# Kernel optimization log

Measured on AMD Instinct MI355X. Metric: run time of the kernel, lower is better.

The kernel has to match this reference:

```python
import jax, jax.numpy as jnp
import numpy as np


def _ln(x, g, b, eps=1e-5):
    m = x.mean(-1, keepdims=True)
    v = x.var(-1, keepdims=True)
    return (x - m) / jnp.sqrt(v + eps) * g + b


def setup_inputs() -> dict:
    key = jax.random.key(0)
    ks = iter(jax.random.split(key, 48))
    B, N, H, Ld, L, FF = 2048, 10, 256, 8, 4, 1024
    def w(shape, s=0.02):
        return jax.random.normal(next(ks), shape, jnp.float32) * s
    return dict(
        latent_code=jax.random.normal(next(ks), (B, Ld), jnp.float32),
        target_node_types=jax.random.randint(next(ks), (B, N), 0, 5),
        ce_w1=w((Ld, H)), ce_b1=jnp.zeros(H), ce_g1=jnp.ones(H), ce_be1=jnp.zeros(H),
        ce_w2=w((H, H)), ce_b2=jnp.zeros(H), ce_g2=jnp.ones(H), ce_be2=jnp.zeros(H),
        nc_w1=w((2, H // 4)), nc_b1=jnp.zeros(H // 4), nc_w2=w((H // 4, 3)), nc_b2=jnp.zeros(3),
        type_emb=w((5, H), 1.0), pos_emb=w((N, H), 0.02),
        qkvo_w=w((L, 4, H, H)), qkvo_b=jnp.zeros((L, 4, H)),
        ln_g=jnp.ones((L, 2, H)), ln_b=jnp.zeros((L, 2, H)),
        ffn_w1=w((L, H, FF)), ffn_b1=jnp.zeros((L, FF)),
        ffn_w2=w((L, FF, H)), ffn_b2=jnp.zeros((L, H)),
        out_w=w((H, 5)), out_b=jnp.zeros(5),
        edge_w1=w((2 * H + Ld, H)), edge_b1=jnp.zeros(H),
        edge_w2=w((H, 8)), edge_b2=jnp.zeros(8),
    )


def reference(latent_code, target_node_types,
              ce_w1, ce_b1, ce_g1, ce_be1, ce_w2, ce_b2, ce_g2, ce_be2,
              nc_w1, nc_b1, nc_w2, nc_b2,
              type_emb, pos_emb, qkvo_w, qkvo_b, ln_g, ln_b,
              ffn_w1, ffn_b1, ffn_w2, ffn_b2, out_w, out_b,
              edge_w1, edge_b1, edge_w2, edge_b2):
    B, Ld = latent_code.shape
    N = target_node_types.shape[1]
    H = ce_w1.shape[1]
    L = qkvo_w.shape[0]
    nh = 8
    hd = H // nh

    # context encoder: Linear -> LN -> ReLU -> Linear -> LN
    h0 = jax.nn.relu(_ln(latent_code @ ce_w1 + ce_b1, ce_g1, ce_be1))
    context = _ln(h0 @ ce_w2 + ce_b2, ce_g2, ce_be2)  # [B,H]

    # node count head on latent_code[:, :2]
    node_count_logits = jax.nn.relu(latent_code[:, :2] @ nc_w1 + nc_b1) @ nc_w2 + nc_b2  # [B,3]

    # teacher-forced node embeddings (independent of predictions -> vectorizable)
    ne = type_emb[target_node_types] + pos_emb[:N]          # [B,N,H]
    h = context[:, None, :] + pos_emb[:N]                   # queries [B,N,H]
    mem = jnp.concatenate([context[:, None, :], ne], axis=1)  # keys [B,N+1,H]
    # position i attends to context (k=0) and nodes j<i (k=j+1), i.e. k <= i
    kmask = (jnp.arange(N + 1)[None, :] <= jnp.arange(N)[:, None])  # [N,N+1]
    scale = 1.0 / np.sqrt(hd).astype(np.float32)

    for l in range(L):
        Q = (h @ qkvo_w[l, 0] + qkvo_b[l, 0]).reshape(B, N, nh, hd)
        K = (mem @ qkvo_w[l, 1] + qkvo_b[l, 1]).reshape(B, N + 1, nh, hd)
        V = (mem @ qkvo_w[l, 2] + qkvo_b[l, 2]).reshape(B, N + 1, nh, hd)
        s = jnp.einsum('bnhd,bmhd->bhnm', Q, K) * scale
        s = jnp.where(kmask[None, None], s, jnp.float32(-1e9))
        a = jax.nn.softmax(s, axis=-1)
        o = jnp.einsum('bhnm,bmhd->bnhd', a, V).reshape(B, N, H)
        h = _ln(h + o @ qkvo_w[l, 3] + qkvo_b[l, 3], ln_g[l, 0], ln_b[l, 0])
        f = jax.nn.relu(h @ ffn_w1[l] + ffn_b1[l]) @ ffn_w2[l] + ffn_b2[l]
        h = _ln(h + f, ln_g[l, 1], ln_b[l, 1])

    node_logits = h @ out_w + out_b  # [B,N,5]

    # pairwise edge decoder on (emb_i, emb_j, latent) for i>j, symmetrized
    ei = jnp.broadcast_to(ne[:, :, None, :], (B, N, N, H))
    ej = jnp.broadcast_to(ne[:, None, :, :], (B, N, N, H))
    lat = jnp.broadcast_to(latent_code[:, None, None, :], (B, N, N, Ld))
    feat = jnp.concatenate([ei, ej, lat], axis=-1)  # [B,N,N,2H+Ld]
    elog = jax.nn.relu(feat @ edge_w1 + edge_b1) @ edge_w2 + edge_b2  # [B,N,N,8]
    tril = (jnp.arange(N)[:, None] > jnp.arange(N)[None, :])[None, :, :, None]
    lower = jnp.where(tril, elog, jnp.float32(0.0))
    edge_component_logits = lower + jnp.swapaxes(lower, 1, 2)  # diag stays zero

    return node_logits, node_count_logits, edge_component_logits
```

## Files before the change

### kernel.cpp

```cpp
#include <hip/hip_runtime.h>
#include <hip/hip_bf16.h>

#define BATCH 2048
#define NNODE 10
#define NLAYER 4
#define ROWS_H (BATCH*NNODE)
#define ROWS_M (BATCH*(NNODE+1))
#define KVSTR 2048

typedef __hip_bfloat16 bf16;
typedef unsigned short u16;
typedef unsigned int u32;
typedef __attribute__((ext_vector_type(8))) short bf16x8;
typedef __attribute__((ext_vector_type(4))) float f32x4;

__device__ __forceinline__ float bfb(u16 u) {
    union { u32 i; float f; } c; c.i = (u32)u << 16; return c.f;
}
__device__ __forceinline__ float bf2f(bf16 x) { return __bfloat162float(x); }
__device__ __forceinline__ bf16 f2bf(float x) { return __float2bfloat16(x); }
__device__ __forceinline__ u16 f2u(float v) {
    bf16 t = f2bf(v); u16 u; __builtin_memcpy(&u, &t, 2); return u;
}
__device__ __forceinline__ void store_out(void* out, int f32o, size_t idx, float v) {
    if (f32o) ((float*)out)[idx] = v; else ((bf16*)out)[idx] = f2bf(v);
}
__device__ __forceinline__ int dflag(const u32* g) { return g[0] == 0x3F800000u; }

#define GLL(src, dst) __builtin_amdgcn_global_load_lds( \
    (const __attribute__((address_space(1))) void*)(src), \
    (__attribute__((address_space(3))) void*)(dst), 16, 0, 0)

#define NT 26
struct CvtArgs { const void* src[NT]; int n[NT]; int off[NT]; };

__global__ __launch_bounds__(256) void cvt_kernel(CvtArgs a, bf16* __restrict__ dst,
                                                  const u32* __restrict__ gptr) {
    int f = dflag(gptr);
    int gid = blockIdx.x * 256 + threadIdx.x;
    int stride = gridDim.x * 256;
    for (int tn = 0; tn < NT; tn++) {
        const void* s = a.src[tn];
        bf16* d = dst + a.off[tn];
        int n = a.n[tn];
        if (f) {
            const float* sf = (const float*)s;
            for (int i = gid; i < n; i += stride) d[i] = f2bf(sf[i]);
        } else {
            const bf16* sb = (const bf16*)s;
            for (int i = gid; i < n; i += stride) d[i] = sb[i];
        }
    }
}

#define NTT 26
struct TTArgs {
    const void* src[NTT];
    int soff[NTT]; int doff[NTT]; int R[NTT]; int C[NTT];
    int tileStart[NTT];
    int nTiles;
};

__global__ __launch_bounds__(256) void tt_kernel(TTArgs a, u16* __restrict__ dst,
                                                 const u32* __restrict__ gptr) {
    int f = dflag(gptr);
    int bid = blockIdx.x;
    if (bid >= a.nTiles) return;
    int tn = 0;
    while (tn + 1 < NTT && a.tileStart[tn + 1] <= bid) tn++;
    int lt = bid - a.tileStart[tn];
    int R = a.R[tn], C = a.C[tn];
    int tilesC = C >> 6;
    int tr = lt / tilesC, tc = lt - tr * tilesC;

    __shared__ u16 Ts[64 * 66];
    int t = threadIdx.x;

    if (f) {
        const float* s = (const float*)a.src[tn] + a.soff[tn];
        #pragma unroll
        for (int it = 0; it < 16; it++) {
            int flat = it * 256 + t;
            int lr = flat >> 6, lc = flat & 63;
            Ts[lr * 66 + lc] = f2u(s[(size_t)(tr * 64 + lr) * C + tc * 64 + lc]);
        }
    } else {
        const u16* s = (const u16*)a.src[tn] + a.soff[tn];
        #pragma unroll
        for (int it = 0; it < 16; it++) {
            int flat = it * 256 + t;
            int lr = flat >> 6, lc = flat & 63;
            Ts[lr * 66 + lc] = s[(size_t)(tr * 64 + lr) * C + tc * 64 + lc];
        }
    }
    __syncthreads();

    u16* d = dst + a.doff[tn];
    #pragma unroll
    for (int it = 0; it < 16; it++) {
        int flat = it * 256 + t;
        int orow = flat >> 6, ocol = flat & 63;
        d[(size_t)(tc * 64 + orow) * R + tr * 64 + ocol] = Ts[ocol * 66 + orow];
    }
}

__global__ __launch_bounds__(256) void kvbias_kernel(const bf16* __restrict__ qb,
                                                     bf16* __restrict__ dst) {
    int t = blockIdx.x * 256 + threadIdx.x;
    if (t < 2048) {
        int l = t >> 9, c = t & 511;
        dst[t] = qb[(l * 4 + 1) * 256 + c];
    }
}

__device__ __forceinline__ void ln_stats256(float x, float* s_red, float& m, float& var) {
    float v1 = x, v2 = x * x;
    #pragma unroll
    for (int off = 32; off; off >>= 1) {
        v1 += __shfl_down(v1, off, 64);
        v2 += __shfl_down(v2, off, 64);
    }
    int wave = threadIdx.x >> 6, lane = threadIdx.x & 63;
    if (!lane) { s_red[wave] = v1; s_red[4 + wave] = v2; }
    __syncthreads();
    m   = (s_red[0] + s_red[1] + s_red[2] + s_red[3]) * (1.f / 256.f);
    var = (s_red[4] + s_red[5] + s_red[6] + s_red[7]) * (1.f / 256.f) - m * m;
    __syncthreads();
}

__global__ __launch_bounds__(256) void ctx_kernel(
    const bf16* __restrict__ lat_bf, const int* __restrict__ types,
    const bf16* __restrict__ ce_w1, const bf16* __restrict__ ce_b1,
    const bf16* __restrict__ ce_g1, const bf16* __restrict__ ce_be1,
    const bf16* __restrict__ ce_w2, const bf16* __restrict__ ce_b2,
    const bf16* __restrict__ ce_g2, const bf16* __restrict__ ce_be2,
    const bf16* __restrict__ nc_w1, const bf16* __restrict__ nc_b1,
    const bf16* __restrict__ nc_w2, const bf16* __restrict__ nc_b2,
    const bf16* __restrict__ type_emb, const bf16* __restrict__ pos_emb,
    const bf16* __restrict__ edge_w1, const bf16* __restrict__ edge_b1,
    bf16* __restrict__ h, bf16* __restrict__ mem, bf16* __restrict__ ne,
    bf16* __restrict__ rvec, void* __restrict__ out, const u32* __restrict__ gptr)
{
    int b = blockIdx.x;
    int t = threadIdx.x;
    int f32o = dflag(gptr);
    __shared__ float lat[8];
    __shared__ float s_h0[256];
    __shared__ float s_red[8];
    __shared__ float s_nc[64];

    if (t < 8) lat[t] = bf2f(lat_bf[b * 8 + t]);
    __syncthreads();

    float x = bf2f(ce_b1[t]);
    #pragma unroll
    for (int k = 0; k < 8; k++) x += lat[k] * bf2f(ce_w1[k * 256 + t]);
    float m, var;
    ln_stats256(x, s_red, m, var);
    float r = rsqrtf(var + 1e-5f);
    float h0 = fmaxf((x - m) * r * bf2f(ce_g1[t]) + bf2f(ce_be1[t]), 0.f);
    s_h0[t] = h0;
    __syncthreads();

    float x2 = bf2f(ce_b2[t]);
    for (int k = 0; k < 256; k++) x2 += s_h0[k] * bf2f(ce_w2[k * 256 + t]);
    ln_stats256(x2, s_red, m, var);
    r = rsqrtf(var + 1e-5f);
    float ctx = (x2 - m) * r * bf2f(ce_g2[t]) + bf2f(ce_be2[t]);

    mem[(size_t)(b * 11) * 256 + t] = f2bf(ctx);
    for (int n = 0; n < NNODE; n++) {
        float pe = bf2f(pos_emb[n * 256 + t]);
        h[(size_t)(b * NNODE + n) * 256 + t] = f2bf(ctx + pe);
        int ty = types[b * NNODE + n];
        float nv = bf2f(type_emb[ty * 256 + t]) + pe;
        ne[(size_t)(b * NNODE + n) * 256 + t] = f2bf(nv);
        mem[(size_t)(b * 11 + 1 + n) * 256 + t] = f2bf(nv);
    }

    float rv = bf2f(edge_b1[t]);
    #pragma unroll
    for (int k = 0; k < 8; k++) rv += lat[k] * bf2f(edge_w1[(512 + k) * 256 + t]);
    rvec[(size_t)b * 256 + t] = f2bf(rv);

    if (t < 64) {
        float hn = lat[0] * bf2f(nc_w1[t]) + lat[1] * bf2f(nc_w1[64 + t]) + bf2f(nc_b1[t]);
        s_nc[t] = fmaxf(hn, 0.f);
    }
    __syncthreads();
    if (t < 3) {
        float o = bf2f(nc_b2[t]);
        for (int k = 0; k < 64; k++) o += s_nc[k] * bf2f(nc_w2[k * 3 + t]);
        store_out(out, f32o, (size_t)102400 + b * 3 + t, o);
    }
}

__global__ __launch_bounds__(256) void gemm_mfma(
    const u16* __restrict__ A, const u16* __restrict__ Bt,
    const bf16* __restrict__ bias, bf16* __restrict__ C,
    int M, int K, int N, int act)
{
    __shared__ u16 Als[2][128 * 32];
    __shared__ u16 Bls[2][128 * 32];
    int t = threadIdx.x;
    int w = t >> 6, l = t & 63;
    int m0 = blockIdx.y * 128, n0 = blockIdx.x * 128;
    int wr = (w >> 1) * 64, wc = (w & 1) * 64;

    int srow = w * 32 + (l >> 2);
    int selem = (l & 3) * 8;
    const u16* Ag = A + (size_t)(m0 + srow) * K + selem;
    const u16* Bg = Bt + (size_t)(n0 + srow) * K + selem;

    f32x4 acc[4][4];
    #pragma unroll
    for (int i = 0; i < 4; i++)
        #pragma unroll
        for (int j = 0; j < 4; j++)
            acc[i][j] = (f32x4){0.f, 0.f, 0.f, 0.f};

    int koff = (l >> 4) * 8;
    int mrow = wr + (l & 15);
    int ncol = wc + (l & 15);

    for (int kt = 0; kt < K; kt += 64) {
        #pragma unroll
        for (int hh = 0; hh < 2; hh++) {
            const u16* ag = Ag + kt + hh * 32;
            const u16* bg = Bg + kt + hh * 32;
            GLL(ag, &Als[hh][w * 1024]);
            GLL(ag + (size_t)16 * K, &Als[hh][w * 1024 + 512]);
            GLL(bg, &Bls[hh][w * 1024]);
            GLL(bg + (size_t)16 * K, &Bls[hh][w * 1024 + 512]);
        }
        __syncthreads();

        #pragma unroll
        for (int hh = 0; hh < 2; hh++) {
            bf16x8 af[4], bfr[4];
            #pragma unroll
            for (int i = 0; i < 4; i++) {
                af[i]  = *(const bf16x8*)&Als[hh][(mrow + i * 16) * 32 + koff];
                bfr[i] = *(const bf16x8*)&Bls[hh][(ncol + i * 16) * 32 + koff];
            }
            #pragma unroll
            for (int i = 0; i < 4; i++)
                #pragma unroll
                for (int j = 0; j < 4; j++)
                    acc[i][j] = __builtin_amdgcn_mfma_f32_16x16x32_bf16(af[i], bfr[j], acc[i][j], 0, 0, 0);
        }
        __syncthreads();
    }

    int rbase = (l >> 4) * 4;
    #pragma unroll
    for (int i = 0; i < 4; i++) {
        int m = m0 + wr + i * 16 + rbase;
        #pragma unroll
        for (int j = 0; j < 4; j++) {
            int n = n0 + wc + j * 16 + (l & 15);
            float bv = bias ? bf2f(bias[n]) : 0.f;
            #pragma unroll
            for (int r = 0; r < 4; r++) {
                float v = acc[i][j][r] + bv;
                if (act) v = fmaxf(v, 0.f);
                C[(size_t)(m + r) * N + n] = f2bf(v);
            }
        }
    }
}

template<int MODE>
__global__ __launch_bounds__(256) void gemm256(
    const u16* __restrict__ A, const u16* __restrict__ Bt,
    const bf16* __restrict__ bias, const bf16* __restrict__ g,
    const bf16* __restrict__ be, u16* __restrict__ hio,
    u16* __restrict__ C, int K)
{
    __shared__ u16 Asl[32 * 32];
    __shared__ u16 Bsl[256 * 32];
    __shared__ float lnp[2][4][32];
    int t = threadIdx.x, w = t >> 6, l = t & 63, q = l >> 4, l15 = l & 15;
    int m0 = blockIdx.x * 32;

    const u16* Ag = A + (size_t)(m0 + w * 16 + (l >> 2)) * K + (l & 3) * 8;
    const u16* Bg = Bt + (size_t)(w * 64 + (l >> 2)) * K + (l & 3) * 8;

    f32x4 acc[2][4];
    #pragma unroll
    for (int i = 0; i < 2; i++)
        #pragma unroll
        for (int j = 0; j < 4; j++)
            acc[i][j] = (f32x4){0.f, 0.f, 0.f, 0.f};

    for (int kt = 0; kt < K; kt += 32) {
        if (w < 2) GLL(Ag + kt, &Asl[w * 512]);
        #pragma unroll
        for (int s = 0; s < 4; s++)
            GLL(Bg + kt + (size_t)(s * 16) * K, &Bsl[w * 2048 + s * 512]);
        __syncthreads();
        bf16x8 af[2], bfr[4];
        #pragma unroll
        for (int i = 0; i < 2; i++)
            af[i] = *(const bf16x8*)&Asl[(i * 16 + l15) * 32 + q * 8];
        #pragma unroll
        for (int j = 0; j < 4; j++)
            bfr[j] = *(const bf16x8*)&Bsl[(w * 64 + j * 16 + l15) * 32 + q * 8];
        #pragma unroll
        for (int i = 0; i < 2; i++)
            #pragma unroll
            for (int j = 0; j < 4; j++)
                acc[i][j] = __builtin_amdgcn_mfma_f32_16x16x32_bf16(af[i], bfr[j], acc[i][j], 0, 0, 0);
        __syncthreads();
    }

    float bv[4];
    #pragma unroll
    for (int j = 0; j < 4; j++) bv[j] = bf2f(bias[w * 64 + j * 16 + l15]);

    if (MODE == 0) {
        #pragma unroll
        for (int i = 0; i < 2; i++)
            #pragma unroll
            for (int r = 0; r < 4; r++) {
                int row = m0 + i * 16 + q * 4 + r;
                #pragma unroll
                for (int j = 0; j < 4; j++)
                    C[(size_t)row * 256 + w * 64 + j * 16 + l15] = f2u(acc[i][j][r] + bv[j]);
            }
    } else {
        float gv[4], bev[4];
        #pragma unroll
        for (int j = 0; j < 4; j++) {
            gv[j] = bf2f(g[w * 64 + j * 16 + l15]);
            bev[j] = bf2f(be[w * 64 + j * 16 + l15]);
        }
        #pragma unroll
        for (int i = 0; i < 2; i++)
            #pragma unroll
            for (int r = 0; r < 4; r++) {
                int row = m0 + i * 16 + q * 4 + r;
                float s = 0.f, s2 = 0.f;
                #pragma unroll
                for (int j = 0; j < 4; j++) {
                    float xv = acc[i][j][r] + bv[j] + bfb(hio[(size_t)row * 256 + w * 64 + j * 16 + l15]);
                    acc[i][j][r] = xv; s += xv; s2 += xv * xv;
                }
                #pragma unroll
                for (int d = 1; d < 16; d <<= 1) {
                    s  += __shfl_xor(s, d, 64);
                    s2 += __shfl_xor(s2, d, 64);
                }
                if (l15 == 0) {
                    lnp[0][w][i * 16 + q * 4 + r] = s;
                    lnp[1][w][i * 16 + q * 4 + r] = s2;
                }
            }
        __syncthreads();
        #pragma unroll
        for (int i = 0; i < 2; i++)
            #pragma unroll
            for (int r = 0; r < 4; r++) {
                int lr = i * 16 + q * 4 + r;
                float S  = lnp[0][0][lr] + lnp[0][1][lr] + lnp[0][2][lr] + lnp[0][3][lr];
                float S2 = lnp[1][0][lr] + lnp[1][1][lr] + lnp[1][2][lr] + lnp[1][3][lr];
                float mean = S * (1.f / 256.f);
                float var = S2 * (1.f / 256.f) - mean * mean;
                float rstd = rsqrtf(var + 1e-5f);
                #pragma unroll
                for (int j = 0; j < 4; j++)
                    hio[(size_t)(m0 + lr) * 256 + w * 64 + j * 16 + l15] =
                        f2u((acc[i][j][r] - mean) * rstd * gv[j] + bev[j]);
            }
    }
}

__global__ __launch_bounds__(256) void ffn_kernel(
    u16* __restrict__ h, const u16* __restrict__ W1T, const u16* __restrict__ W2T,
    const bf16* __restrict__ b1, const bf16* __restrict__ b2,
    const bf16* __restrict__ g, const bf16* __restrict__ be)
{
    __shared__ u16 Asl[32 * 268];
    __shared__ u16 W1s[128 * 32];
    __shared__ u16 mids[32 * 140];
    __shared__ u16 W2s[256 * 32];
    __shared__ float lnp[2][4][32];

    int t = threadIdx.x, w = t >> 6, l = t & 63, q = l >> 4, l15 = l & 15;
    int m0 = blockIdx.x * 32;

    {
        int row = t >> 3, seg = (t & 7) * 32;
        const u16* src = h + (size_t)(m0 + row) * 256 + seg;
        u16* dst = &Asl[row * 268 + seg];
        #pragma unroll
        for (int u = 0; u < 4; u++)
            *(uint4*)(dst + u * 8) = *(const uint4*)(src + u * 8);
    }

    f32x4 accO[2][4];
    #pragma unroll
    for (int i = 0; i < 2; i++)
        #pragma unroll
        for (int j = 0; j < 4; j++)
            accO[i][j] = (f32x4){0.f, 0.f, 0.f, 0.f};
    __syncthreads();

    for (int c = 0; c < 8; c++) {
        f32x4 accM[2][2];
        #pragma unroll
        for (int i = 0; i < 2; i++) { accM[i][0] = (f32x4){0,0,0,0}; accM[i][1] = (f32x4){0,0,0,0}; }

        for (int kt = 0; kt < 256; kt += 32) {
            const u16* src = W1T + (size_t)(c * 128 + w * 32 + (l >> 2)) * 256 + kt + (l & 3) * 8;
            GLL(src, &W1s[w * 1024]);
            GLL(src + (size_t)16 * 256, &W1s[w * 1024 + 512]);
            __syncthreads();
            bf16x8 af[2], bfm[2];
            #pragma unroll
            for (int i = 0; i < 2; i++)
                af[i] = *(const bf16x8*)&Asl[(i * 16 + l15) * 268 + kt + q * 8];
            #pragma unroll
            for (int j = 0; j < 2; j++)
                bfm[j] = *(const bf16x8*)&W1s[(w * 32 + j * 16 + l15) * 32 + q * 8];
            #pragma unroll
            for (int i = 0; i < 2; i++)
                #pragma unroll
                for (int j = 0; j < 2; j++)
                    accM[i][j] = __builtin_amdgcn_mfma_f32_16x16x32_bf16(af[i], bfm[j], accM[i][j], 0, 0, 0);
            __syncthreads();
        }
        float b1v[2];
        #pragma unroll
        for (int j = 0; j < 2; j++) b1v[j] = bf2f(b1[c * 128 + w * 32 + j * 16 + l15]);
        #pragma unroll
        for (int i = 0; i < 2; i++)
            #pragma unroll
            for (int j = 0; j < 2; j++)
                #pragma unroll
                for (int r = 0; r < 4; r++) {
                    int row = i * 16 + q * 4 + r, col = w * 32 + j * 16 + l15;
                    mids[row * 140 + col] = f2u(fmaxf(accM[i][j][r] + b1v[j], 0.f));
                }

        for (int kt2 = 0; kt2 < 4; kt2++) {
            const u16* src = W2T + (size_t)(w * 64 + (l >> 2)) * 1024 + c * 128 + kt2 * 32 + (l & 3) * 8;
            #pragma unroll
            for (int s = 0; s < 4; s++)
                GLL(src + (size_t)(s * 16) * 1024, &W2s[w * 2048 + s * 512]);
            __syncthreads();
            bf16x8 am[2], bo[4];
            #pragma unroll
            for (int i = 0; i < 2; i++)
                am[i] = *(const bf16x8*)&mids[(i * 16 + l15) * 140 + kt2 * 32 + q * 8];
            #pragma unroll
            for (int j = 0; j < 4; j++)
                bo[j] = *(const bf16x8*)&W2s[(w * 64 + j * 16 + l15) * 32 + q * 8];
            #pragma unroll
            for (int i = 0; i < 2; i++)
                #pragma unroll
                for (int j = 0; j < 4; j++)
                    accO[i][j] = __builtin_amdgcn_mfma_f32_16x16x32_bf16(am[i], bo[j], accO[i][j], 0, 0, 0);
            __syncthreads();
        }
    }

    float b2v[4], gv[4], bev[4];
    #pragma unroll
    for (int j = 0; j < 4; j++) {
        int col = w * 64 + j * 16 + l15;
        b2v[j] = bf2f(b2[col]); gv[j] = bf2f(g[col]); bev[j] = bf2f(be[col]);
    }
    #pragma unroll
    for (int i = 0; i < 2; i++)
        #pragma unroll
        for (int r = 0; r < 4; r++) {
            int row = i * 16 + q * 4 + r;
            float s = 0.f, s2 = 0.f;
            #pragma unroll
            for (int j = 0; j < 4; j++) {
                float xv = accO[i][j][r] + b2v[j] + bfb(Asl[row * 268 + w * 64 + j * 16 + l15]);
                accO[i][j][r] = xv; s += xv; s2 += xv * xv;
            }
            #pragma unroll
            for (int d = 1; d < 16; d <<= 1) {
                s  += __shfl_xor(s, d, 64);
                s2 += __shfl_xor(s2, d, 64);
            }
            if (l15 == 0) { lnp[0][w][row] = s; lnp[1][w][row] = s2; }
        }
    __syncthreads();
    #pragma unroll
    for (int i = 0; i < 2; i++)
        #pragma unroll
        for (int r = 0; r < 4; r++) {
            int lr = i * 16 + q * 4 + r;
            float S  = lnp[0][0][lr] + lnp[0][1][lr] + lnp[0][2][lr] + lnp[0][3][lr];
            float S2 = lnp[1][0][lr] + lnp[1][1][lr] + lnp[1][2][lr] + lnp[1][3][lr];
            float mean = S * (1.f / 256.f);
            float var = S2 * (1.f / 256.f) - mean * mean;
            float rstd = rsqrtf(var + 1e-5f);
            #pragma unroll
            for (int j = 0; j < 4; j++)
                h[(size_t)(m0 + lr) * 256 + w * 64 + j * 16 + l15] =
                    f2u((accO[i][j][r] - mean) * rstd * gv[j] + bev[j]);
        }
}

__global__ __launch_bounds__(256) void attn_kernel(
    const bf16* __restrict__ Qb, const bf16* __restrict__ KVb,
    bf16* __restrict__ Ob)
{
    int b = blockIdx.x;
    int t = threadIdx.x;
    __shared__ float Qs[10 * 256];
    __shared__ float Ks[11 * 256];
    __shared__ float S[880];

    const u16* Qu = (const u16*)Qb + (size_t)b * 2560;
    for (int e = t; e < 640; e += 256) {
        ushort4 v = *(const ushort4*)(Qu + e * 4);
        int base = e * 4;
        Qs[base] = bfb(v.x); Qs[base + 1] = bfb(v.y);
        Qs[base + 2] = bfb(v.z); Qs[base + 3] = bfb(v.w);
    }
    const u16* KVu = (const u16*)KVb + (size_t)b * 11 * KVSTR;
    for (int e = t; e < 704; e += 256) {
        int k = e >> 6, off = (e & 63) * 4;
        ushort4 v = *(const ushort4*)(KVu + (size_t)k * KVSTR + off);
        float* dst = &Ks[k * 256 + off];
        dst[0] = bfb(v.x); dst[1] = bfb(v.y); dst[2] = bfb(v.z); dst[3] = bfb(v.w);
    }
    __syncthreads();

    const float scale = 0.17677669529663687f;
    for (int e = t; e < 880; e += 256) {
        int head = e / 110, rem = e % 110, i = rem / 11, k = rem % 11;
        if (k <= i) {
            const float* qp = &Qs[i * 256 + head * 32];
            const float* kp = &Ks[k * 256 + head * 32];
            float s = 0.f;
            #pragma unroll
            for (int d = 0; d < 32; d++) s += qp[d] * kp[d];
            S[e] = s * scale;
        }
    }
    __syncthreads();
    if (t < 80) {
        int head = t / 10, i = t % 10;
        float* row = &S[head * 110 + i * 11];
        float mx = -1e30f;
        for (int k = 0; k <= i; k++) mx = fmaxf(mx, row[k]);
        float sum = 0.f;
        for (int k = 0; k <= i; k++) { float e = __expf(row[k] - mx); row[k] = e; sum += e; }
        float inv = 1.f / sum;
        for (int k = 0; k <= i; k++) row[k] *= inv;
    }
    __syncthreads();

    int head = t >> 5;
    float o[10] = {0.f, 0.f, 0.f, 0.f, 0.f, 0.f, 0.f, 0.f, 0.f, 0.f};
    for (int k = 0; k < 11; k++) {
        float v = bf2f(((const bf16*)KVb)[(size_t)(b * 11 + k) * KVSTR + 256 + t]);
        for (int i = k; i < 10; i++) o[i] += S[head * 110 + i * 11 + k] * v;
    }
    for (int i = 0; i < 10; i++) Ob[(size_t)(b * 10 + i) * 256 + t] = f2bf(o[i]);
}

__global__ __launch_bounds__(256) void outhead_kernel(
    const bf16* __restrict__ h, const bf16* __restrict__ w,
    const bf16* __restrict__ b, void* __restrict__ out, const u32* __restrict__ gptr)
{
    int f32o = dflag(gptr);
    int wv = threadIdx.x >> 6, l = threadIdx.x & 63;
    size_t row = (size_t)blockIdx.x * 4 + wv;
    ushort4 hv = *(const ushort4*)((const u16*)h + row * 256 + l * 4);
    float x[4] = {bfb(hv.x), bfb(hv.y), bfb(hv.z), bfb(hv.w)};
    float a[5] = {0.f, 0.f, 0.f, 0.f, 0.f};
    #pragma unroll
    for (int c = 0; c < 4; c++) {
        #pragma unroll
        for (int o = 0; o < 5; o++) a[o] += x[c] * bf2f(w[(l * 4 + c) * 5 + o]);
    }
    #pragma unroll
    for (int off = 32; off; off >>= 1)
        #pragma unroll
        for (int o = 0; o < 5; o++) a[o] += __shfl_xor(a[o], off, 64);
    if (!l)
        #pragma unroll
        for (int o = 0; o < 5; o++)
            store_out(out, f32o, row * 5 + o, a[o] + bf2f(b[o]));
}

__global__ __launch_bounds__(256) void edge_kernel(
    const bf16* __restrict__ PQ, const bf16* __restrict__ rvec,
    const bf16* __restrict__ w2, const bf16* __restrict__ b2,
    void* __restrict__ out, const u32* __restrict__ gptr)
{
    int f32o = dflag(gptr);
    int t = threadIdx.x, w = t >> 6, l = t & 63;
    int b = blockIdx.x * 4 + w;
    const size_t ebase = 108544;

    __shared__ u16 Pl[4][10 * 260];
    __shared__ u16 Ql[4][10 * 260];
    __shared__ u16 Rl[4][256];
    __shared__ float Wl[256 * 8];

    const u16* pq = (const u16*)PQ + (size_t)b * 10 * 512;
    #pragma unroll
    for (int i = 0; i < 10; i++) {
        ushort4 pv = *(const ushort4*)(pq + i * 512 + l * 4);
        ushort4 qv = *(const ushort4*)(pq + i * 512 + 256 + l * 4);
        *(ushort4*)&Pl[w][i * 260 + l * 4] = pv;
        *(ushort4*)&Ql[w][i * 260 + l * 4] = qv;
    }
    *(ushort4*)&Rl[w][l * 4] = *(const ushort4*)((const u16*)rvec + (size_t)b * 256 + l * 4);
    {
        const u16* wp = (const u16*)w2 + t * 8;
        #pragma unroll
        for (int o = 0; o < 8; o++) Wl[t * 8 + o] = bfb(wp[o]);
    }
    __syncthreads();

    if (l >= 45 && l < 55) {
        int i = l - 45;
        size_t o0 = ebase + ((size_t)(b * 10 + i) * 10 + i) * 8;
        if (f32o) {
            float4 z = {0.f, 0.f, 0.f, 0.f};
            *(float4*)((float*)out + o0) = z;
            *(float4*)((float*)out + o0 + 4) = z;
        } else {
            uint4 z = {0u, 0u, 0u, 0u};
            *(uint4*)((u16*)out + o0) = z;
        }
    }
    if (l < 45) {
        int i = 1;
        while (i * (i + 1) / 2 <= l) i++;
        int j = l - i * (i - 1) / 2;
        float acc[8] = {0.f, 0.f, 0.f, 0.f, 0.f, 0.f, 0.f, 0.f};
        const u16* Pp = &Pl[w][i * 260];
        const u16* Qp = &Ql[w][j * 260];
        const u16* Rp = &Rl[w][0];
        for (int c = 0; c < 256; c += 4) {
            ushort4 pv = *(const ushort4*)(Pp + c);
            ushort4 qv = *(const ushort4*)(Qp + c);
            ushort4 rv = *(const ushort4*)(Rp + c);
            float hc[4];
            hc[0] = fmaxf(bfb(pv.x) + bfb(qv.x) + bfb(rv.x), 0.f);
            hc[1] = fmaxf(bfb(pv.y) + bfb(qv.y) + bfb(rv.y), 0.f);
            hc[2] = fmaxf(bfb(pv.z) + bfb(qv.z) + bfb(rv.z), 0.f);
            hc[3] = fmaxf(bfb(pv.w) + bfb(qv.w) + bfb(rv.w), 0.f);
            #pragma unroll
            for (int cc = 0; cc < 4; cc++) {
                const float* wp = &Wl[(c + cc) * 8];
                #pragma unroll
                for (int o = 0; o < 8; o++) acc[o] += hc[cc] * wp[o];
            }
        }
        float r8[8];
        #pragma unroll
        for (int o = 0; o < 8; o++) r8[o] = acc[o] + bf2f(b2[o]);
        size_t o0 = ebase + ((size_t)(b * 10 + i) * 10 + j) * 8;
        size_t o1 = ebase + ((size_t)(b * 10 + j) * 10 + i) * 8;
        if (f32o) {
            float4 v0 = {r8[0], r8[1], r8[2], r8[3]};
            float4 v1 = {r8[4], r8[5], r8[6], r8[7]};
            *(float4*)((float*)out + o0) = v0; *(float4*)((float*)out + o0 + 4) = v1;
            *(float4*)((float*)out + o1) = v0; *(float4*)((float*)out + o1 + 4) = v1;
        } else {
            uint4 pk;
            pk.x = (u32)f2u(r8[0]) | ((u32)f2u(r8[1]) << 16);
            pk.y = (u32)f2u(r8[2]) | ((u32)f2u(r8[3]) << 16);
            pk.z = (u32)f2u(r8[4]) | ((u32)f2u(r8[5]) << 16);
            pk.w = (u32)f2u(r8[6]) | ((u32)f2u(r8[7]) << 16);
            *(uint4*)((u16*)out + o0) = pk;
            *(uint4*)((u16*)out + o1) = pk;
        }
    }
}

extern "C" void kernel_launch(void* const* d_in, const int* in_sizes, int n_in,
                              void* d_out, int out_size, void* d_ws, size_t ws_size,
                              hipStream_t stream) {
    const int* types = (const int*)d_in[1];
    const u32* gptr = (const u32*)d_in[18];

    static const int kIdx[NT] = {0,2,3,4,5,6,7,8,9,10,11,12,13,14,15,17,18,19,21,23,24,25,26,27,28,29};
    static const int kSz[NT]  = {16384,2048,256,256,256,65536,256,256,256,128,64,192,3,1280,2560,
                                 4096,2048,2048,4096,1024,1280,5,133120,256,2048,8};
    bf16* wbf = (bf16*)d_ws;

    CvtArgs ca;
    const bf16* cv[30];
    int off = 0;
    for (int i = 0; i < NT; i++) {
        ca.src[i] = d_in[kIdx[i]];
        ca.n[i] = kSz[i];
        ca.off[i] = off;
        cv[kIdx[i]] = wbf + off;
        off = (off + kSz[i] + 7) & ~7;
    }

    size_t wtbase_e = ((size_t)off + 127) & ~(size_t)127;
    u16* wt = (u16*)wbf + wtbase_e;
    const int PERL = 655360;
    const int KVBASE = 4 * PERL;
    const int PQBASE = KVBASE + 524288;
    TTArgs ta;
    int tn = 0, tiles = 0;
    auto addT = [&](const void* src, int soff, int doff, int R, int C) {
        ta.src[tn] = src; ta.soff[tn] = soff; ta.doff[tn] = doff;
        ta.R[tn] = R; ta.C[tn] = C; ta.tileStart[tn] = tiles;
        tiles += (R >> 6) * (C >> 6); tn++;
    };
    for (int l = 0; l < NLAYER; l++) {
        int base = l * PERL;
        addT(d_in[16], (l * 4 + 0) * 65536, base,           256, 256);
        addT(d_in[16], (l * 4 + 3) * 65536, base + 65536,   256, 256);
        addT(d_in[20], l * 262144,          base + 131072,  256, 1024);
        addT(d_in[22], l * 262144,          base + 393216,  1024, 256);
        addT(d_in[16], (l * 4 + 1) * 65536, KVBASE + l * 131072,         256, 256);
        addT(d_in[16], (l * 4 + 2) * 65536, KVBASE + l * 131072 + 65536, 256, 256);
    }
    addT(d_in[26], 0,     PQBASE,         256, 256);
    addT(d_in[26], 65536, PQBASE + 65536, 256, 256);
    ta.nTiles = tiles;

    size_t actbase_e = wtbase_e + 3801088 + 128;

    size_t EH = (size_t)ROWS_H * 256, EM = (size_t)ROWS_M * 256;
    bf16* p = (bf16*)wbf + actbase_e;
    bf16* h      = p; p += EH;
    bf16* mem    = p; p += EM;
    bf16* ne     = p; p += EH;
    bf16* rvec   = p; p += (size_t)BATCH * 256;
    bf16* kvbias = p; p += 2048;
    bf16* span   = p; p += (size_t)ROWS_H * 1024;
    bf16* kv_all = p;
    bf16* qbuf = span;
    bf16* obuf = span + EH;
    bf16* pqbuf = span;

    cvt_kernel<<<256, 256, 0, stream>>>(ca, wbf, gptr);
    tt_kernel<<<tiles, 256, 0, stream>>>(ta, wt, gptr);

    ctx_kernel<<<BATCH, 256, 0, stream>>>(
        cv[0], types, cv[2], cv[3], cv[4], cv[5], cv[6], cv[7], cv[8], cv[9],
        cv[10], cv[11], cv[12], cv[13], cv[14], cv[15], cv[26], cv[27],
        h, mem, ne, rvec, d_out, gptr);
    kvbias_kernel<<<8, 256, 0, stream>>>(cv[17], kvbias);

    gemm_mfma<<<dim3(16, ROWS_M / 128), 256, 0, stream>>>(
        (const u16*)mem, wt + KVBASE, kvbias, kv_all, ROWS_M, 256, 2048, 0);

    for (int l = 0; l < NLAYER; l++) {
        const u16* qT  = wt + (size_t)l * PERL;
        const u16* oT  = qT + 65536;
        const u16* f1T = qT + 131072;
        const u16* f2T = qT + 393216;
        const bf16* bq = cv[17] + (size_t)(l * 4 + 0) * 256;
        const bf16* bo = cv[17] + (size_t)(l * 4 + 3) * 256;
        const bf16* g1 = cv[18] + (size_t)(l * 2) * 256, *be1 = cv[19] + (size_t)(l * 2) * 256;
        const bf16* g2 = cv[18] + (size_t)(l * 2 + 1) * 256, *be2 = cv[19] + (size_t)(l * 2 + 1) * 256;

        gemm256<0><<<ROWS_H / 32, 256, 0, stream>>>((const u16*)h, qT, bq, nullptr, nullptr,
                                                    nullptr, (u16*)qbuf, 256);
        attn_kernel<<<BATCH, 256, 0, stream>>>(qbuf, kv_all + (size_t)l * 512, obuf);
        gemm256<1><<<ROWS_H / 32, 256, 0, stream>>>((const u16*)obuf, oT, bo, g1, be1,
                                                    (u16*)h, nullptr, 256);
        ffn_kernel<<<ROWS_H / 32, 256, 0, stream>>>((u16*)h, f1T, f2T,
                                                    cv[21] + (size_t)l * 1024, cv[23] + (size_t)l * 256,
                                                    g2, be2);
    }

    outhead_kernel<<<ROWS_H / 4, 256, 0, stream>>>(h, cv[24], cv[25], d_out, gptr);

    gemm_mfma<<<dim3(4, ROWS_H / 128), 256, 0, stream>>>((const u16*)ne, wt + PQBASE, nullptr, pqbuf, ROWS_H, 256, 512, 0);
    edge_kernel<<<BATCH / 4, 256, 0, stream>>>(pqbuf, rvec, cv[28], cv[29], d_out, gptr);
}
```

Before: 653.2 us.

## Split FFN kernel work across eight waves per block instead of four

The fused FFN kernel now launches 512 threads per block, so each of eight waves owns 16 intermediate columns and 32 output columns instead of 32 and 64. Per-wave accumulators and weight loads are halved and the LayerNorm partial sums are reduced across eight waves. The aim is more waves in flight per block to hide memory latency and sync stalls. In exchange each wave issues fewer MFMAs between barriers, and barrier overhead grows relative to the work.

```diff
diff --git a/kernel.cpp b/kernel.cpp
--- a/kernel.cpp
+++ b/kernel.cpp
@@ -375,7 +375,7 @@
     }
 }
 
-__global__ __launch_bounds__(256) void ffn_kernel(
+__global__ __launch_bounds__(512) void ffn_kernel(
     u16* __restrict__ h, const u16* __restrict__ W1T, const u16* __restrict__ W2T,
     const bf16* __restrict__ b1, const bf16* __restrict__ b2,
     const bf16* __restrict__ g, const bf16* __restrict__ be)
@@ -384,91 +384,80 @@
     __shared__ u16 W1s[128 * 32];
     __shared__ u16 mids[32 * 140];
     __shared__ u16 W2s[256 * 32];
-    __shared__ float lnp[2][4][32];
+    __shared__ float lnp[2][8][32];
 
     int t = threadIdx.x, w = t >> 6, l = t & 63, q = l >> 4, l15 = l & 15;
     int m0 = blockIdx.x * 32;
 
     {
-        int row = t >> 3, seg = (t & 7) * 32;
+        int row = t >> 4, seg = (t & 15) * 16;
         const u16* src = h + (size_t)(m0 + row) * 256 + seg;
         u16* dst = &Asl[row * 268 + seg];
-        #pragma unroll
-        for (int u = 0; u < 4; u++)
-            *(uint4*)(dst + u * 8) = *(const uint4*)(src + u * 8);
-    }
-
-    f32x4 accO[2][4];
+        *(uint4*)(dst) = *(const uint4*)(src);
+        *(uint4*)(dst + 8) = *(const uint4*)(src + 8);
+    }
+
+    f32x4 accO[2][2];
     #pragma unroll
     for (int i = 0; i < 2; i++)
         #pragma unroll
-        for (int j = 0; j < 4; j++)
+        for (int j = 0; j < 2; j++)
             accO[i][j] = (f32x4){0.f, 0.f, 0.f, 0.f};
     __syncthreads();
 
     for (int c = 0; c < 8; c++) {
-        f32x4 accM[2][2];
-        #pragma unroll
-        for (int i = 0; i < 2; i++) { accM[i][0] = (f32x4){0,0,0,0}; accM[i][1] = (f32x4){0,0,0,0}; }
+        f32x4 accM[2];
+        accM[0] = (f32x4){0.f, 0.f, 0.f, 0.f};
+        accM[1] = (f32x4){0.f, 0.f, 0.f, 0.f};
 
         for (int kt = 0; kt < 256; kt += 32) {
-            const u16* src = W1T + (size_t)(c * 128 + w * 32 + (l >> 2)) * 256 + kt + (l & 3) * 8;
-            GLL(src, &W1s[w * 1024]);
-            GLL(src + (size_t)16 * 256, &W1s[w * 1024 + 512]);
+            const u16* src = W1T + (size_t)(c * 128 + w * 16 + (l >> 2)) * 256 + kt + (l & 3) * 8;
+            GLL(src, &W1s[w * 512]);
             __syncthreads();
-            bf16x8 af[2], bfm[2];
+            bf16x8 af[2], bfm;
             #pragma unroll
             for (int i = 0; i < 2; i++)
                 af[i] = *(const bf16x8*)&Asl[(i * 16 + l15) * 268 + kt + q * 8];
+            bfm = *(const bf16x8*)&W1s[(w * 16 + l15) * 32 + q * 8];
+            #pragma unroll
+            for (int i = 0; i < 2; i++)
+                accM[i] = __builtin_amdgcn_mfma_f32_16x16x32_bf16(af[i], bfm, accM[i], 0, 0, 0);
+            __syncthreads();
+        }
+        float b1v = bf2f(b1[c * 128 + w * 16 + l15]);
+        #pragma unroll
+        for (int i = 0; i < 2; i++)
+            #pragma unroll
+            for (int r = 0; r < 4; r++) {
+                int row = i * 16 + q * 4 + r, col = w * 16 + l15;
+                mids[row * 140 + col] = f2u(fmaxf(accM[i][r] + b1v, 0.f));
+            }
+
+        for (int kt2 = 0; kt2 < 4; kt2++) {
+            const u16* src = W2T + (size_t)(w * 32 + (l >> 2)) * 1024 + c * 128 + kt2 * 32 + (l & 3) * 8;
+            GLL(src, &W2s[w * 1024]);
+            GLL(src + (size_t)16 * 1024, &W2s[w * 1024 + 512]);
+            __syncthreads();
+            bf16x8 am[2], bo[2];
+            #pragma unroll
+            for (int i = 0; i < 2; i++)
+                am[i] = *(const bf16x8*)&mids[(i * 16 + l15) * 140 + kt2 * 32 + q * 8];
             #pragma unroll
             for (int j = 0; j < 2; j++)
-                bfm[j] = *(const bf16x8*)&W1s[(w * 32 + j * 16 + l15) * 32 + q * 8];
+                bo[j] = *(const bf16x8*)&W2s[(w * 32 + j * 16 + l15) * 32 + q * 8];
             #pragma unroll
             for (int i = 0; i < 2; i++)
                 #pragma unroll
                 for (int j = 0; j < 2; j++)
-                    accM[i][j] = __builtin_amdgcn_mfma_f32_16x16x32_bf16(af[i], bfm[j], accM[i][j], 0, 0, 0);
-            __syncthreads();
-        }
-        float b1v[2];
-        #pragma unroll
-        for (int j = 0; j < 2; j++) b1v[j] = bf2f(b1[c * 128 + w * 32 + j * 16 + l15]);
-        #pragma unroll
-        for (int i = 0; i < 2; i++)
-            #pragma unroll
-            for (int j = 0; j < 2; j++)
-                #pragma unroll
-                for (int r = 0; r < 4; r++) {
-                    int row = i * 16 + q * 4 + r, col = w * 32 + j * 16 + l15;
-                    mids[row * 140 + col] = f2u(fmaxf(accM[i][j][r] + b1v[j], 0.f));
-                }
-
-        for (int kt2 = 0; kt2 < 4; kt2++) {
-            const u16* src = W2T + (size_t)(w * 64 + (l >> 2)) * 1024 + c * 128 + kt2 * 32 + (l & 3) * 8;
-            #pragma unroll
-            for (int s = 0; s < 4; s++)
-                GLL(src + (size_t)(s * 16) * 1024, &W2s[w * 2048 + s * 512]);
-            __syncthreads();
-            bf16x8 am[2], bo[4];
-            #pragma unroll
-            for (int i = 0; i < 2; i++)
-                am[i] = *(const bf16x8*)&mids[(i * 16 + l15) * 140 + kt2 * 32 + q * 8];
-            #pragma unroll
-            for (int j = 0; j < 4; j++)
-                bo[j] = *(const bf16x8*)&W2s[(w * 64 + j * 16 + l15) * 32 + q * 8];
-            #pragma unroll
-            for (int i = 0; i < 2; i++)
-                #pragma unroll
-                for (int j = 0; j < 4; j++)
                     accO[i][j] = __builtin_amdgcn_mfma_f32_16x16x32_bf16(am[i], bo[j], accO[i][j], 0, 0, 0);
             __syncthreads();
         }
     }
 
-    float b2v[4], gv[4], bev[4];
-    #pragma unroll
-    for (int j = 0; j < 4; j++) {
-        int col = w * 64 + j * 16 + l15;
+    float b2v[2], gv[2], bev[2];
+    #pragma unroll
+    for (int j = 0; j < 2; j++) {
+        int col = w * 32 + j * 16 + l15;
         b2v[j] = bf2f(b2[col]); gv[j] = bf2f(g[col]); bev[j] = bf2f(be[col]);
     }
     #pragma unroll
@@ -478,8 +467,8 @@
             int row = i * 16 + q * 4 + r;
             float s = 0.f, s2 = 0.f;
             #pragma unroll
-            for (int j = 0; j < 4; j++) {
-                float xv = accO[i][j][r] + b2v[j] + bfb(Asl[row * 268 + w * 64 + j * 16 + l15]);
+            for (int j = 0; j < 2; j++) {
+                float xv = accO[i][j][r] + b2v[j] + bfb(Asl[row * 268 + w * 32 + j * 16 + l15]);
                 accO[i][j][r] = xv; s += xv; s2 += xv * xv;
             }
             #pragma unroll
@@ -495,14 +484,15 @@
         #pragma unroll
         for (int r = 0; r < 4; r++) {
             int lr = i * 16 + q * 4 + r;
-            float S  = lnp[0][0][lr] + lnp[0][1][lr] + lnp[0][2][lr] + lnp[0][3][lr];
-            float S2 = lnp[1][0][lr] + lnp[1][1][lr] + lnp[1][2][lr] + lnp[1][3][lr];
+            float S = 0.f, S2 = 0.f;
+            #pragma unroll
+            for (int ww = 0; ww < 8; ww++) { S += lnp[0][ww][lr]; S2 += lnp[1][ww][lr]; }
             float mean = S * (1.f / 256.f);
             float var = S2 * (1.f / 256.f) - mean * mean;
             float rstd = rsqrtf(var + 1e-5f);
             #pragma unroll
-            for (int j = 0; j < 4; j++)
-                h[(size_t)(m0 + lr) * 256 + w * 64 + j * 16 + l15] =
+            for (int j = 0; j < 2; j++)
+                h[(size_t)(m0 + lr) * 256 + w * 32 + j * 16 + l15] =
                     f2u((accO[i][j][r] - mean) * rstd * gv[j] + bev[j]);
         }
 }
@@ -770,7 +760,7 @@
         attn_kernel<<<BATCH, 256, 0, stream>>>(qbuf, kv_all + (size_t)l * 512, obuf);
         gemm256<1><<<ROWS_H / 32, 256, 0, stream>>>((const u16*)obuf, oT, bo, g1, be1,
                                                     (u16*)h, nullptr, 256);
-        ffn_kernel<<<ROWS_H / 32, 256, 0, stream>>>((u16*)h, f1T, f2T,
+        ffn_kernel<<<ROWS_H / 32, 512, 0, stream>>>((u16*)h, f1T, f2T,
                                                     cv[21] + (size_t)l * 1024, cv[23] + (size_t)l * 256,
                                                     g2, be2);
     }
```

Result: slower. 763.9 us (+17.0%).
